# Kernel tuning notes

Measured on AMD Instinct MI355X. Metric: run time of the kernel, lower is better.

Reference implementation:

```python
import jax, jax.numpy as jnp
import numpy as np

TEMP = 0.1  # simclr_temp


def setup_inputs() -> dict:
    key = jax.random.key(0)
    features = jax.random.normal(key, (4096, 512), dtype=jnp.float32)
    return {"features": features}


def reference(features):
    N, d = features.shape
    B = N // 2

    # L2-normalize rows (torch F.normalize, eps=1e-12)
    norm = jnp.maximum(jnp.linalg.norm(features, axis=1, keepdims=True), 1e-12)
    f = features / norm

    # dense cosine-similarity matrix [N, N]
    sim = f @ f.T

    # static index bookkeeping (numpy, known at trace time)
    idx = np.arange(N)
    pos_col = (idx + B) % N  # the other view of the same image

    # positives: sim[i, (i+B) % N], shape [N, 1]
    pos = sim[jnp.arange(N), jnp.asarray(pos_col)][:, None]

    # negatives: all columns except the diagonal and the positive, ascending
    # order per row, exactly matching torch's ~mask .view reshapes -> [N, N-2]
    full = np.broadcast_to(idx, (N, N))
    keep = (full != idx[:, None]) & (full != pos_col[:, None])
    neg_cols = jnp.asarray(full[keep].reshape(N, N - 2))
    neg = jnp.take_along_axis(sim, neg_cols, axis=1)

    logits = jnp.concatenate([pos, neg], axis=1) / TEMP  # [N, N-1]

    # cross-entropy with target class 0 for every row
    loss = jnp.mean(jax.nn.logsumexp(logits, axis=1) - logits[:, 0])
    return loss
```

## Files before the change

### kernel.cpp

```cpp
#include <hip/hip_runtime.h>
#include <hip/hip_bf16.h>

typedef unsigned short u16;
typedef __attribute__((ext_vector_type(8))) short short8;
typedef __attribute__((ext_vector_type(4))) float f32x4;

#define NROWS 4096
#define DIM   512
#define TINV  10.0f

__device__ __forceinline__ u16 f2bf(float x) {
    unsigned u = __float_as_uint(x);
    unsigned r = (u + 0x7FFFu + ((u >> 16) & 1u)) >> 16;
    return (u16)r;
}

__global__ __launch_bounds__(256) void k_norm(const float* __restrict__ in,
                                              u16* __restrict__ out) {
    const int row  = blockIdx.x * 4 + (threadIdx.x >> 6);
    const int lane = threadIdx.x & 63;
    const float* rp = in + (size_t)row * DIM;

    float4 v0 = ((const float4*)rp)[lane];
    float4 v1 = ((const float4*)rp)[lane + 64];

    float ssq = v0.x*v0.x + v0.y*v0.y + v0.z*v0.z + v0.w*v0.w
              + v1.x*v1.x + v1.y*v1.y + v1.z*v1.z + v1.w*v1.w;
    #pragma unroll
    for (int m = 32; m; m >>= 1) ssq += __shfl_xor(ssq, m);

    const float scale = 1.0f / fmaxf(sqrtf(ssq), 1e-12f);

    u16* op = out + (size_t)row * DIM;
    u16 o0[4], o1[4];
    o0[0] = f2bf(v0.x * scale); o0[1] = f2bf(v0.y * scale);
    o0[2] = f2bf(v0.z * scale); o0[3] = f2bf(v0.w * scale);
    o1[0] = f2bf(v1.x * scale); o1[1] = f2bf(v1.y * scale);
    o1[2] = f2bf(v1.z * scale); o1[3] = f2bf(v1.w * scale);
    ((ushort4*)op)[lane]      = make_ushort4(o0[0], o0[1], o0[2], o0[3]);
    ((ushort4*)op)[lane + 64] = make_ushort4(o1[0], o1[1], o1[2], o1[3]);
}

__device__ __forceinline__ void gload_lds16(const u16* g, u16* l) {
    __builtin_amdgcn_global_load_lds(
        (const __attribute__((address_space(1))) void*)g,
        (__attribute__((address_space(3))) void*)l, 16, 0, 0);
}

__global__ __launch_bounds__(256) void k_gemm(const u16* __restrict__ fb,
                                              float* __restrict__ S,
                                              float* __restrict__ P) {
    __shared__ u16 lA[128 * 32];
    __shared__ u16 lB[128 * 32];

    const int tid  = threadIdx.x;
    const int lane = tid & 63;
    const int wid  = tid >> 6;
    const int wr   = wid >> 1;
    const int wc   = wid & 1;
    const int brow = blockIdx.y * 128;
    const int bcol = blockIdx.x * 128;

    const int lr = lane & 15;
    const int kg = lane >> 4;

    f32x4 acc[4][4];
    #pragma unroll
    for (int m = 0; m < 4; ++m)
        #pragma unroll
        for (int n = 0; n < 4; ++n)
            acc[m][n] = (f32x4){0.f, 0.f, 0.f, 0.f};

    for (int kk = 0; kk < DIM; kk += 32) {
        #pragma unroll
        for (int i = 0; i < 2; ++i) {
            const int c = tid + i * 256;
            const int r = c >> 2;
            const int o = (c & 3) * 8;
            gload_lds16(fb + (size_t)(brow + r) * DIM + kk + o, lA + c * 8);
            gload_lds16(fb + (size_t)(bcol + r) * DIM + kk + o, lB + c * 8);
        }
        __syncthreads();

        short8 a[4], b[4];
        #pragma unroll
        for (int m = 0; m < 4; ++m)
            a[m] = *(const short8*)&lA[(wr * 64 + m * 16 + lr) * 32 + kg * 8];
        #pragma unroll
        for (int n = 0; n < 4; ++n)
            b[n] = *(const short8*)&lB[(wc * 64 + n * 16 + lr) * 32 + kg * 8];

        #pragma unroll
        for (int m = 0; m < 4; ++m)
            #pragma unroll
            for (int n = 0; n < 4; ++n)
                acc[m][n] = __builtin_amdgcn_mfma_f32_16x16x32_bf16(
                    a[m], b[n], acc[m][n], 0, 0, 0);
        __syncthreads();
    }

    #pragma unroll
    for (int m = 0; m < 4; ++m) {
        #pragma unroll
        for (int r = 0; r < 4; ++r) {
            const int grow = brow + wr * 64 + m * 16 + kg * 4 + r;
            float rs = 0.f;
            #pragma unroll
            for (int n = 0; n < 4; ++n) {
                const int gcol = bcol + wc * 64 + n * 16 + lr;
                const float s = acc[m][n][r];
                if (gcol == (grow ^ 2048)) P[grow] = s;
                const float e = (gcol == grow) ? 0.f : __expf(TINV * (s - 1.0f));
                rs += e;
            }
            rs += __shfl_xor(rs, 1);
            rs += __shfl_xor(rs, 2);
            rs += __shfl_xor(rs, 4);
            rs += __shfl_xor(rs, 8);
            if (lr == 0) atomicAdd(&S[grow], rs);
        }
    }
}

__global__ __launch_bounds__(256) void k_final(const float* __restrict__ S,
                                               const float* __restrict__ P,
                                               float* __restrict__ out) {
    __shared__ float red[256];
    float local = 0.f;
    for (int r = threadIdx.x; r < NROWS; r += 256)
        local += TINV + logf(S[r]) - TINV * P[r];
    red[threadIdx.x] = local;
    __syncthreads();
    #pragma unroll
    for (int s = 128; s; s >>= 1) {
        if (threadIdx.x < s) red[threadIdx.x] += red[threadIdx.x + s];
        __syncthreads();
    }
    if (threadIdx.x == 0) out[0] = red[0] * (1.0f / NROWS);
}

extern "C" void kernel_launch(void* const* d_in, const int* in_sizes, int n_in,
                              void* d_out, int out_size, void* d_ws, size_t ws_size,
                              hipStream_t stream) {
    const float* feat = (const float*)d_in[0];

    u16*   fb = (u16*)d_ws;
    float* S  = (float*)((char*)d_ws + (size_t)NROWS * DIM * 2);
    float* P  = S + NROWS;

    hipMemsetAsync(S, 0, NROWS * sizeof(float), stream);
    k_norm<<<NROWS / 4, 256, 0, stream>>>(feat, fb);
    k_gemm<<<dim3(32, 32), 256, 0, stream>>>(fb, S, P);
    k_final<<<1, 256, 0, stream>>>(S, P, (float*)d_out);
}
```

Before: 103.7 us.

## Exploit Gram symmetry, widen K tile with swizzled LDS, fold memset into norm

The GEMM now computes only upper-triangular 128x128 tiles and uses the symmetry of f f^T. Each off-diagonal tile adds both row sums and column sums of exp terms into S, and the positive pair is written for both rows. Diagonal tiles load one LDS buffer, and the K step is doubled to 64 with an XOR-swizzled LDS layout to reduce bank conflicts and halve the number of barriers. The memset is folded into the norm kernel and the final reduction uses 1024 threads. Together this roughly halves the MFMA and exp work. The costs are more atomics, idle early-exit blocks, and load imbalance across the grid.

```diff
diff --git a/kernel.cpp b/kernel.cpp
--- a/kernel.cpp
+++ b/kernel.cpp
@@ -16,11 +16,13 @@
 }
 
 __global__ __launch_bounds__(256) void k_norm(const float* __restrict__ in,
-                                              u16* __restrict__ out) {
+                                              u16* __restrict__ out,
+                                              float* __restrict__ S) {
     const int row  = blockIdx.x * 4 + (threadIdx.x >> 6);
     const int lane = threadIdx.x & 63;
+    if (threadIdx.x < 4) S[blockIdx.x * 4 + threadIdx.x] = 0.f;
+
     const float* rp = in + (size_t)row * DIM;
-
     float4 v0 = ((const float4*)rp)[lane];
     float4 v1 = ((const float4*)rp)[lane + 64];
 
@@ -32,13 +34,12 @@
     const float scale = 1.0f / fmaxf(sqrtf(ssq), 1e-12f);
 
     u16* op = out + (size_t)row * DIM;
-    u16 o0[4], o1[4];
-    o0[0] = f2bf(v0.x * scale); o0[1] = f2bf(v0.y * scale);
-    o0[2] = f2bf(v0.z * scale); o0[3] = f2bf(v0.w * scale);
-    o1[0] = f2bf(v1.x * scale); o1[1] = f2bf(v1.y * scale);
-    o1[2] = f2bf(v1.z * scale); o1[3] = f2bf(v1.w * scale);
-    ((ushort4*)op)[lane]      = make_ushort4(o0[0], o0[1], o0[2], o0[3]);
-    ((ushort4*)op)[lane + 64] = make_ushort4(o1[0], o1[1], o1[2], o1[3]);
+    ((ushort4*)op)[lane] = make_ushort4(
+        f2bf(v0.x * scale), f2bf(v0.y * scale),
+        f2bf(v0.z * scale), f2bf(v0.w * scale));
+    ((ushort4*)op)[lane + 64] = make_ushort4(
+        f2bf(v1.x * scale), f2bf(v1.y * scale),
+        f2bf(v1.z * scale), f2bf(v1.w * scale));
 }
 
 __device__ __forceinline__ void gload_lds16(const u16* g, u16* l) {
@@ -50,19 +51,23 @@
 __global__ __launch_bounds__(256) void k_gemm(const u16* __restrict__ fb,
                                               float* __restrict__ S,
                                               float* __restrict__ P) {
-    __shared__ u16 lA[128 * 32];
-    __shared__ u16 lB[128 * 32];
+    const int br = blockIdx.y, bc = blockIdx.x;
+    if (bc < br) return;
+    const bool diag = (br == bc);
+    const bool posT = (bc == (br ^ 16));
+
+    __shared__ u16 lA[128 * 64];
+    __shared__ u16 lB[128 * 64];
 
     const int tid  = threadIdx.x;
     const int lane = tid & 63;
     const int wid  = tid >> 6;
     const int wr   = wid >> 1;
     const int wc   = wid & 1;
-    const int brow = blockIdx.y * 128;
-    const int bcol = blockIdx.x * 128;
-
-    const int lr = lane & 15;
-    const int kg = lane >> 4;
+    const int brow = br * 128;
+    const int bcol = bc * 128;
+    const int lr   = lane & 15;
+    const int kg   = lane >> 4;
 
     f32x4 acc[4][4];
     #pragma unroll
@@ -71,34 +76,59 @@
         for (int n = 0; n < 4; ++n)
             acc[m][n] = (f32x4){0.f, 0.f, 0.f, 0.f};
 
-    for (int kk = 0; kk < DIM; kk += 32) {
+    const u16* Bsrc = diag ? lA : lB;
+
+    for (int kk = 0; kk < DIM; kk += 64) {
         #pragma unroll
-        for (int i = 0; i < 2; ++i) {
-            const int c = tid + i * 256;
-            const int r = c >> 2;
-            const int o = (c & 3) * 8;
-            gload_lds16(fb + (size_t)(brow + r) * DIM + kk + o, lA + c * 8);
-            gload_lds16(fb + (size_t)(bcol + r) * DIM + kk + o, lB + c * 8);
+        for (int i = 0; i < 4; ++i) {
+            const int q  = tid + i * 256;
+            const int r  = q >> 3;
+            const int c  = q & 7;
+            const int sc = c ^ (r & 7);
+            gload_lds16(fb + (size_t)(brow + r) * DIM + kk + sc * 8, lA + q * 8);
+        }
+        if (!diag) {
+            #pragma unroll
+            for (int i = 0; i < 4; ++i) {
+                const int q  = tid + i * 256;
+                const int r  = q >> 3;
+                const int c  = q & 7;
+                const int sc = c ^ (r & 7);
+                gload_lds16(fb + (size_t)(bcol + r) * DIM + kk + sc * 8, lB + q * 8);
+            }
         }
         __syncthreads();
 
-        short8 a[4], b[4];
+        short8 a[4][2], b[4][2];
         #pragma unroll
-        for (int m = 0; m < 4; ++m)
-            a[m] = *(const short8*)&lA[(wr * 64 + m * 16 + lr) * 32 + kg * 8];
+        for (int m = 0; m < 4; ++m) {
+            const int row = wr * 64 + m * 16 + lr;
+            #pragma unroll
+            for (int ks = 0; ks < 2; ++ks)
+                a[m][ks] = *(const short8*)
+                    &lA[row * 64 + (((ks * 4 + kg) ^ (row & 7)) * 8)];
+        }
         #pragma unroll
-        for (int n = 0; n < 4; ++n)
-            b[n] = *(const short8*)&lB[(wc * 64 + n * 16 + lr) * 32 + kg * 8];
+        for (int n = 0; n < 4; ++n) {
+            const int row = wc * 64 + n * 16 + lr;
+            #pragma unroll
+            for (int ks = 0; ks < 2; ++ks)
+                b[n][ks] = *(const short8*)
+                    &Bsrc[row * 64 + (((ks * 4 + kg) ^ (row & 7)) * 8)];
+        }
 
         #pragma unroll
-        for (int m = 0; m < 4; ++m)
+        for (int ks = 0; ks < 2; ++ks)
             #pragma unroll
-            for (int n = 0; n < 4; ++n)
-                acc[m][n] = __builtin_amdgcn_mfma_f32_16x16x32_bf16(
-                    a[m], b[n], acc[m][n], 0, 0, 0);
+            for (int m = 0; m < 4; ++m)
+                #pragma unroll
+                for (int n = 0; n < 4; ++n)
+                    acc[m][n] = __builtin_amdgcn_mfma_f32_16x16x32_bf16(
+                        a[m][ks], b[n][ks], acc[m][n], 0, 0, 0);
         __syncthreads();
     }
 
+    float cs[4] = {0.f, 0.f, 0.f, 0.f};
     #pragma unroll
     for (int m = 0; m < 4; ++m) {
         #pragma unroll
@@ -109,9 +139,11 @@
             for (int n = 0; n < 4; ++n) {
                 const int gcol = bcol + wc * 64 + n * 16 + lr;
                 const float s = acc[m][n][r];
-                if (gcol == (grow ^ 2048)) P[grow] = s;
-                const float e = (gcol == grow) ? 0.f : __expf(TINV * (s - 1.0f));
+                if (posT && gcol == (grow ^ 2048)) { P[grow] = s; P[gcol] = s; }
+                float e = __expf(TINV * (s - 1.0f));
+                if (diag && gcol == grow) e = 0.f;
                 rs += e;
+                if (!diag) cs[n] += e;
             }
             rs += __shfl_xor(rs, 1);
             rs += __shfl_xor(rs, 2);
@@ -120,19 +152,31 @@
             if (lr == 0) atomicAdd(&S[grow], rs);
         }
     }
+    if (!diag) {
+        #pragma unroll
+        for (int n = 0; n < 4; ++n) {
+            cs[n] += __shfl_xor(cs[n], 16);
+            cs[n] += __shfl_xor(cs[n], 32);
+            if (kg == 0)
+                atomicAdd(&S[bcol + wc * 64 + n * 16 + lr], cs[n]);
+        }
+    }
 }
 
-__global__ __launch_bounds__(256) void k_final(const float* __restrict__ S,
-                                               const float* __restrict__ P,
-                                               float* __restrict__ out) {
-    __shared__ float red[256];
+__global__ __launch_bounds__(1024) void k_final(const float* __restrict__ S,
+                                                const float* __restrict__ P,
+                                                float* __restrict__ out) {
+    __shared__ float red[1024];
     float local = 0.f;
-    for (int r = threadIdx.x; r < NROWS; r += 256)
+    #pragma unroll
+    for (int i = 0; i < 4; ++i) {
+        const int r = threadIdx.x + i * 1024;
         local += TINV + logf(S[r]) - TINV * P[r];
+    }
     red[threadIdx.x] = local;
     __syncthreads();
     #pragma unroll
-    for (int s = 128; s; s >>= 1) {
+    for (int s = 512; s; s >>= 1) {
         if (threadIdx.x < s) red[threadIdx.x] += red[threadIdx.x + s];
         __syncthreads();
     }
@@ -148,8 +192,7 @@
     float* S  = (float*)((char*)d_ws + (size_t)NROWS * DIM * 2);
     float* P  = S + NROWS;
 
-    hipMemsetAsync(S, 0, NROWS * sizeof(float), stream);
-    k_norm<<<NROWS / 4, 256, 0, stream>>>(feat, fb);
+    k_norm<<<NROWS / 4, 256, 0, stream>>>(feat, fb, S);
     k_gemm<<<dim3(32, 32), 256, 0, stream>>>(fb, S, P);
-    k_final<<<1, 256, 0, stream>>>(S, P, (float*)d_out);
+    k_final<<<1, 1024, 0, stream>>>(S, P, (float*)d_out);
 }
```

After: 88.95 us. 14.2% less time.
